# Optimization experiments

Hardware: AMD Instinct MI355X
Metric: run time of the kernel (lower is better)

Reference implementation:

```python
import jax, jax.numpy as jnp
import numpy as np

HID = 1024
NEG = -1e10


def setup_inputs() -> dict:
    key = jax.random.key(0)
    ks = jax.random.split(key, 8)
    batch, src_len = 64, 512
    hidden = jax.random.normal(ks[0], (batch, HID), dtype=jnp.float32)
    encoder_outputs = jax.random.normal(ks[1], (src_len, batch, 2 * HID), dtype=jnp.float32)
    mask = jax.random.randint(ks[2], (batch, src_len), 0, 2).astype(bool)
    # params (torch Linear: y = x @ W.T + b)
    sW = 1.0 / np.sqrt(HID)
    sU = 1.0 / np.sqrt(2 * HID)
    W_w = jax.random.uniform(ks[3], (HID, HID), jnp.float32, -sW, sW)
    W_b = jax.random.uniform(ks[4], (HID,), jnp.float32, -sW, sW)
    U_w = jax.random.uniform(ks[5], (HID, 2 * HID), jnp.float32, -sU, sU)
    U_b = jax.random.uniform(ks[6], (HID,), jnp.float32, -sU, sU)
    v_w = jax.random.uniform(ks[7], (1, HID), jnp.float32, -sW, sW)
    return {"hidden": hidden, "encoder_outputs": encoder_outputs, "mask": mask,
            "W_w": W_w, "W_b": W_b, "U_w": U_w, "U_b": U_b, "v_w": v_w}


def reference(hidden, encoder_outputs, mask, W_w, W_b, U_w, U_b, v_w):
    # hidden: [B, H]; encoder_outputs: [S, B, 2H]; mask: [B, S]
    Wh = hidden @ W_w.T + W_b                       # [B, H], broadcast over S
    enc = jnp.transpose(encoder_outputs, (1, 0, 2))  # [B, S, 2H]
    Ue = jnp.einsum('bse,he->bsh', enc, U_w) + U_b   # [B, S, H]
    energy = jnp.tanh(Wh[:, None, :] + Ue) @ v_w[0]  # [B, S]
    energy = jnp.where(mask, NEG, energy)
    return jax.nn.softmax(energy, axis=1)
```

## Files before the change

### kernel.cpp

```cpp
#include <hip/hip_runtime.h>
#include <math.h>

#define HID   1024
#define HID2  2048
#define BATCH 64
#define SRC   512
#define MROWS (SRC * BATCH)
#define NEGV  (-1e10f)

typedef int  i4v __attribute__((ext_vector_type(4)));
typedef float f4v __attribute__((ext_vector_type(4)));

__global__ void zero_energy(float* __restrict__ e) {
    int i = blockIdx.x * 256 + threadIdx.x;
    if (i < MROWS) e[i] = 0.f;
}

__global__ void split_i8(const float* __restrict__ src,
                         signed char* __restrict__ q1b,
                         signed char* __restrict__ q2b,
                         int n16, float s1, float inv_s1, float s2) {
    int i = blockIdx.x * 256 + threadIdx.x;
    if (i >= n16) return;
    const float4* s = (const float4*)src + (size_t)i * 4;
    float v[16];
    *(float4*)&v[0]  = s[0];
    *(float4*)&v[4]  = s[1];
    *(float4*)&v[8]  = s[2];
    *(float4*)&v[12] = s[3];
    unsigned w1[4], w2[4];
#pragma unroll
    for (int p = 0; p < 4; ++p) {
        unsigned a1 = 0, a2 = 0;
#pragma unroll
        for (int j = 0; j < 4; ++j) {
            float a  = v[p * 4 + j];
            float q1 = rintf(a * s1);
            q1 = fminf(fmaxf(q1, -127.f), 127.f);
            float r  = fmaf(q1, -inv_s1, a);
            float q2 = rintf(r * s2);
            q2 = fminf(fmaxf(q2, -127.f), 127.f);
            a1 |= ((unsigned)((int)q1 & 0xff)) << (8 * j);
            a2 |= ((unsigned)((int)q2 & 0xff)) << (8 * j);
        }
        w1[p] = a1; w2[p] = a2;
    }
    ((uint4*)q1b)[i] = make_uint4(w1[0], w1[1], w1[2], w1[3]);
    ((uint4*)q2b)[i] = make_uint4(w2[0], w2[1], w2[2], w2[3]);
}

__global__ void quant_i8(const float* __restrict__ src,
                         signed char* __restrict__ qb,
                         int n16, float s) {
    int i = blockIdx.x * 256 + threadIdx.x;
    if (i >= n16) return;
    const float4* sp = (const float4*)src + (size_t)i * 4;
    float v[16];
    *(float4*)&v[0]  = sp[0];
    *(float4*)&v[4]  = sp[1];
    *(float4*)&v[8]  = sp[2];
    *(float4*)&v[12] = sp[3];
    unsigned w[4];
#pragma unroll
    for (int p = 0; p < 4; ++p) {
        unsigned a = 0;
#pragma unroll
        for (int j = 0; j < 4; ++j) {
            float q = rintf(v[p * 4 + j] * s);
            q = fminf(fmaxf(q, -127.f), 127.f);
            a |= ((unsigned)((int)q & 0xff)) << (8 * j);
        }
        w[p] = a;
    }
    ((uint4*)qb)[i] = make_uint4(w[0], w[1], w[2], w[3]);
}

__global__ void wh_kernel(const float* __restrict__ hidden,
                          const float* __restrict__ W_w,
                          const float* __restrict__ W_b,
                          float* __restrict__ Wh) {
    __shared__ float sh[HID];
    const int b = blockIdx.y;
    const int t = threadIdx.x;
    for (int k = t; k < HID; k += 256) sh[k] = hidden[b * HID + k];
    __syncthreads();
    const int h = blockIdx.x * 256 + t;
    const float* wr = W_w + (size_t)h * HID;
    float acc = 0.f;
    for (int k = 0; k < HID; k += 4) {
        float4 w = *(const float4*)(wr + k);
        acc += sh[k] * w.x + sh[k+1] * w.y + sh[k+2] * w.z + sh[k+3] * w.w;
    }
    Wh[b * HID + h] = acc + W_b[h];
}

static __device__ __forceinline__ float tanh_fast(float x) {
    float ax = fabsf(x);
    float t  = __expf(-2.f * ax);
    float r  = __fdividef(1.f - t, 1.f + t);
    return copysignf(r, x);
}

__global__ __launch_bounds__(256, 2)
void gemm_energy(const signed char* __restrict__ A1,
                 const signed char* __restrict__ A2,
                 const signed char* __restrict__ B1,
                 const float* __restrict__ Ub,
                 const float* __restrict__ vw,
                 const float* __restrict__ Wh,
                 float* __restrict__ energy,
                 int m_base)
{
    __shared__ signed char sAll[2 * 3 * 8192];

    const int tid  = threadIdx.x;
    const int wave = tid >> 6;
    const int lane = tid & 63;

    const int nwg = (int)(gridDim.x * gridDim.y);
    const int bid = (int)(blockIdx.y * gridDim.x + blockIdx.x);
    const int cpx = nwg >> 3;
    const int swz = (bid & 7) * cpx + (bid >> 3);
    const int h0 = (swz & 7) * 128;
    const int m0 = (swz >> 3) * 128;

    const int wm = wave & 1;
    const int wn = wave >> 1;

    i4v c1[4][4], c2[4][4];
#pragma unroll
    for (int i = 0; i < 4; i++)
#pragma unroll
        for (int j = 0; j < 4; j++) {
            c1[i][j] = (i4v){0, 0, 0, 0};
            c2[i][j] = (i4v){0, 0, 0, 0};
        }

    const int ar = lane & 15;
    const int ko = (((lane >> 4) ^ ((ar >> 1) & 3)) * 16);

#define STAGE_TILES(CB, K0)                                                   \
    {                                                                         \
        _Pragma("unroll")                                                     \
        for (int it = 0; it < 2; ++it) {                                      \
            const int f    = it * 256 + tid;                                  \
            const int row  = f >> 2;                                          \
            const int inn  = (((f & 3) ^ ((row >> 1) & 3))) * 16;             \
            const int loff = (CB) + (it * 256 + wave * 64) * 16;              \
            const signed char* ga = A1 + (size_t)(m0 + row) * HID2 + (K0) + inn; \
            __builtin_amdgcn_global_load_lds(                                 \
                (const __attribute__((address_space(1))) unsigned int*)ga,    \
                (__attribute__((address_space(3))) unsigned int*)(sAll + loff), \
                16, 0, 0);                                                    \
            const signed char* gb = A2 + (size_t)(m0 + row) * HID2 + (K0) + inn; \
            __builtin_amdgcn_global_load_lds(                                 \
                (const __attribute__((address_space(1))) unsigned int*)gb,    \
                (__attribute__((address_space(3))) unsigned int*)(sAll + 8192 + loff), \
                16, 0, 0);                                                    \
            const signed char* gc = B1 + (size_t)(h0 + row) * HID2 + (K0) + inn; \
            __builtin_amdgcn_global_load_lds(                                 \
                (const __attribute__((address_space(1))) unsigned int*)gc,    \
                (__attribute__((address_space(3))) unsigned int*)(sAll + 16384 + loff), \
                16, 0, 0);                                                    \
        }                                                                     \
    }

    STAGE_TILES(0, 0);
    asm volatile("s_waitcnt vmcnt(0)" ::: "memory");
    __builtin_amdgcn_s_barrier();

    int cur = 0;
    for (int ks = 0; ks < 32; ++ks) {
        const int cb = cur * 24576;
        if (ks + 1 < 32) STAGE_TILES(cb ^ 24576, (ks + 1) * 64);

        i4v a1[4], a2[4], b1[4];
#pragma unroll
        for (int i = 0; i < 4; ++i) {
            const int ra = cb + (wm * 64 + i * 16 + ar) * 64 + ko;
            const int rb = cb + 16384 + (wn * 64 + i * 16 + ar) * 64 + ko;
            a1[i] = *(const i4v*)&sAll[ra];
            a2[i] = *(const i4v*)&sAll[8192 + ra];
            b1[i] = *(const i4v*)&sAll[rb];
        }
        asm volatile("s_waitcnt lgkmcnt(0)" ::: "memory");
        __builtin_amdgcn_sched_barrier(0);

        __builtin_amdgcn_s_setprio(1);
#pragma unroll
        for (int i = 0; i < 4; ++i)
#pragma unroll
            for (int j = 0; j < 4; ++j) {
                c1[i][j] = __builtin_amdgcn_mfma_i32_16x16x64_i8(a1[i], b1[j], c1[i][j], 0, 0, 0);
                c2[i][j] = __builtin_amdgcn_mfma_i32_16x16x64_i8(a2[i], b1[j], c2[i][j], 0, 0, 0);
            }
        __builtin_amdgcn_s_setprio(0);

        asm volatile("s_waitcnt vmcnt(0)" ::: "memory");
        __builtin_amdgcn_s_barrier();
        cur ^= 1;
    }
#undef STAGE_TILES

    const int col = lane & 15;
    const int rg  = lane >> 4;
    const float invs = 1.f / (4096.f * 5746.f);
    float vj[4], ubj[4];
#pragma unroll
    for (int j = 0; j < 4; ++j) {
        const int hc = h0 + wn * 64 + j * 16 + col;
        vj[j]  = vw[hc];
        ubj[j] = Ub[hc];
    }
#pragma unroll
    for (int i = 0; i < 4; ++i) {
#pragma unroll
        for (int r = 0; r < 4; ++r) {
            const int mm = m0 + wm * 64 + i * 16 + rg * 4 + r;
            const int b  = (m_base + mm) & 63;
            const float* whr = Wh + b * HID + h0 + wn * 64 + col;
            float e = 0.f;
#pragma unroll
            for (int j = 0; j < 4; ++j) {
                float C = fmaf((float)c1[i][j][r], 256.f, (float)c2[i][j][r]) * invs;
                float x = C + ubj[j] + whr[j * 16];
                e += vj[j] * tanh_fast(x);
            }
            e += __shfl_xor(e, 1, 64);
            e += __shfl_xor(e, 2, 64);
            e += __shfl_xor(e, 4, 64);
            e += __shfl_xor(e, 8, 64);
            if (col == 0) atomicAdd(&energy[m_base + mm], e);
        }
    }
}

__global__ void softmax_kernel(const float* __restrict__ energy,
                               const int* __restrict__ mask,
                               float* __restrict__ out) {
    const int b = blockIdx.x;
    const int t = threadIdx.x;
    __shared__ float wmax[4], wsum[4];

    float x0 = energy[t * 64 + b];
    float x1 = energy[(t + 256) * 64 + b];
    float e0 = mask[b * SRC + t]       ? NEGV : x0;
    float e1 = mask[b * SRC + t + 256] ? NEGV : x1;

    float mx = fmaxf(e0, e1);
#pragma unroll
    for (int off = 1; off < 64; off <<= 1)
        mx = fmaxf(mx, __shfl_xor(mx, off, 64));
    const int wid = t >> 6, lane = t & 63;
    if (lane == 0) wmax[wid] = mx;
    __syncthreads();
    mx = fmaxf(fmaxf(wmax[0], wmax[1]), fmaxf(wmax[2], wmax[3]));

    float p0 = expf(e0 - mx), p1 = expf(e1 - mx);
    float sum = p0 + p1;
#pragma unroll
    for (int off = 1; off < 64; off <<= 1)
        sum += __shfl_xor(sum, off, 64);
    if (lane == 0) wsum[wid] = sum;
    __syncthreads();
    sum = wsum[0] + wsum[1] + wsum[2] + wsum[3];
    const float inv = 1.f / sum;
    out[b * SRC + t]       = p0 * inv;
    out[b * SRC + t + 256] = p1 * inv;
}

extern "C" void kernel_launch(void* const* d_in, const int* in_sizes, int n_in,
                              void* d_out, int out_size, void* d_ws, size_t ws_size,
                              hipStream_t stream) {
    const float* hidden = (const float*)d_in[0];
    const float* enc    = (const float*)d_in[1];
    const int*   mask   = (const int*)d_in[2];
    const float* W_w    = (const float*)d_in[3];
    const float* W_b    = (const float*)d_in[4];
    const float* U_w    = (const float*)d_in[5];
    const float* U_b    = (const float*)d_in[6];
    const float* v_w    = (const float*)d_in[7];
    float* out = (float*)d_out;

    char* p = (char*)d_ws;
    float* Wh     = (float*)p;             p += (size_t)BATCH * HID * 4;
    float* energy = (float*)p;             p += (size_t)MROWS * 4;
    signed char* B1 = (signed char*)p;     p += (size_t)HID * HID2;
    const size_t fixed = (size_t)(p - (char*)d_ws);

    int R = 1024;
    const int cand[6] = {32768, 16384, 8192, 4096, 2048, 1024};
    for (int c = 0; c < 6; ++c) {
        if (fixed + (size_t)cand[c] * HID2 * 2 <= ws_size) { R = cand[c]; break; }
    }
    signed char* A1 = (signed char*)p;
    signed char* A2 = A1 + (size_t)R * HID2;

    const float Sa1 = 16.f, iSa1 = 1.f / 16.f, Sa2 = 4096.f;
    const float Sb1 = 5746.f;

    hipLaunchKernelGGL(zero_energy, dim3(MROWS / 256), dim3(256), 0, stream, energy);
    hipLaunchKernelGGL(wh_kernel, dim3(4, BATCH), dim3(256), 0, stream,
                       hidden, W_w, W_b, Wh);
    {
        const int n16 = HID * HID2 / 16;
        hipLaunchKernelGGL(quant_i8, dim3((n16 + 255) / 256), dim3(256), 0, stream,
                           U_w, B1, n16, Sb1);
    }
    for (int c0 = 0; c0 < MROWS; c0 += R) {
        const int n16 = R * HID2 / 16;
        hipLaunchKernelGGL(split_i8, dim3((n16 + 255) / 256), dim3(256), 0, stream,
                           enc + (size_t)c0 * HID2, A1, A2, n16, Sa1, iSa1, Sa2);
        hipLaunchKernelGGL(gemm_energy, dim3(HID / 128, R / 128), dim3(256), 0, stream,
                           A1, A2, B1, U_b, v_w, Wh, energy, c0);
    }
    hipLaunchKernelGGL(softmax_kernel, dim3(BATCH), dim3(256), 0, stream,
                       energy, mask, out);
}
```

Before: 604.0 us.

## Triple-buffer GEMM LDS tiles and use grid-stride coalesced quantization kernels

The int8 GEMM moves from double to triple buffering in shared memory. Tiles are prefetched two K-steps ahead, and the barrier waits with vmcnt(6) so the next stage's loads stay in flight. The setprio and sched_barrier hints are removed. The quantization kernels become grid-stride loops that handle one float4 per thread per iteration with fixed grid sizes, which gives coalesced narrow stores. Raising shared memory to 72KB per block may reduce occupancy below the two blocks per CU that the launch bounds request.

```diff
diff --git a/kernel.cpp b/kernel.cpp
--- a/kernel.cpp
+++ b/kernel.cpp
@@ -19,22 +19,17 @@
 __global__ void split_i8(const float* __restrict__ src,
                          signed char* __restrict__ q1b,
                          signed char* __restrict__ q2b,
-                         int n16, float s1, float inv_s1, float s2) {
-    int i = blockIdx.x * 256 + threadIdx.x;
-    if (i >= n16) return;
-    const float4* s = (const float4*)src + (size_t)i * 4;
-    float v[16];
-    *(float4*)&v[0]  = s[0];
-    *(float4*)&v[4]  = s[1];
-    *(float4*)&v[8]  = s[2];
-    *(float4*)&v[12] = s[3];
-    unsigned w1[4], w2[4];
-#pragma unroll
-    for (int p = 0; p < 4; ++p) {
+                         int n4, float s1, float inv_s1, float s2) {
+    const float4* s4 = (const float4*)src;
+    unsigned* o1 = (unsigned*)q1b;
+    unsigned* o2 = (unsigned*)q2b;
+    for (int i = blockIdx.x * 256 + threadIdx.x; i < n4; i += gridDim.x * 256) {
+        float4 v = s4[i];
+        float vv[4] = {v.x, v.y, v.z, v.w};
         unsigned a1 = 0, a2 = 0;
 #pragma unroll
         for (int j = 0; j < 4; ++j) {
-            float a  = v[p * 4 + j];
+            float a  = vv[j];
             float q1 = rintf(a * s1);
             q1 = fminf(fmaxf(q1, -127.f), 127.f);
             float r  = fmaf(q1, -inv_s1, a);
@@ -43,36 +38,28 @@
             a1 |= ((unsigned)((int)q1 & 0xff)) << (8 * j);
             a2 |= ((unsigned)((int)q2 & 0xff)) << (8 * j);
         }
-        w1[p] = a1; w2[p] = a2;
-    }
-    ((uint4*)q1b)[i] = make_uint4(w1[0], w1[1], w1[2], w1[3]);
-    ((uint4*)q2b)[i] = make_uint4(w2[0], w2[1], w2[2], w2[3]);
+        o1[i] = a1;
+        o2[i] = a2;
+    }
 }
 
 __global__ void quant_i8(const float* __restrict__ src,
                          signed char* __restrict__ qb,
-                         int n16, float s) {
-    int i = blockIdx.x * 256 + threadIdx.x;
-    if (i >= n16) return;
-    const float4* sp = (const float4*)src + (size_t)i * 4;
-    float v[16];
-    *(float4*)&v[0]  = sp[0];
-    *(float4*)&v[4]  = sp[1];
-    *(float4*)&v[8]  = sp[2];
-    *(float4*)&v[12] = sp[3];
-    unsigned w[4];
-#pragma unroll
-    for (int p = 0; p < 4; ++p) {
+                         int n4, float s) {
+    const float4* s4 = (const float4*)src;
+    unsigned* o = (unsigned*)qb;
+    for (int i = blockIdx.x * 256 + threadIdx.x; i < n4; i += gridDim.x * 256) {
+        float4 v = s4[i];
+        float vv[4] = {v.x, v.y, v.z, v.w};
         unsigned a = 0;
 #pragma unroll
         for (int j = 0; j < 4; ++j) {
-            float q = rintf(v[p * 4 + j] * s);
+            float q = rintf(vv[j] * s);
             q = fminf(fmaxf(q, -127.f), 127.f);
             a |= ((unsigned)((int)q & 0xff)) << (8 * j);
         }
-        w[p] = a;
-    }
-    ((uint4*)qb)[i] = make_uint4(w[0], w[1], w[2], w[3]);
+        o[i] = a;
+    }
 }
 
 __global__ void wh_kernel(const float* __restrict__ hidden,
@@ -111,7 +98,7 @@
                  float* __restrict__ energy,
                  int m_base)
 {
-    __shared__ signed char sAll[2 * 3 * 8192];
+    __shared__ signed char sAll[3 * 3 * 8192];
 
     const int tid  = threadIdx.x;
     const int wave = tid >> 6;
@@ -165,28 +152,26 @@
         }                                                                     \
     }
 
+#define SYNC_KEEP6() asm volatile("s_waitcnt vmcnt(6) lgkmcnt(0)\n\ts_barrier" ::: "memory")
+#define SYNC_DRAIN() asm volatile("s_waitcnt vmcnt(0) lgkmcnt(0)\n\ts_barrier" ::: "memory")
+
     STAGE_TILES(0, 0);
-    asm volatile("s_waitcnt vmcnt(0)" ::: "memory");
-    __builtin_amdgcn_s_barrier();
-
-    int cur = 0;
+    STAGE_TILES(24576, 64);
+    SYNC_KEEP6();
+
+    int pv = 2 * 24576, cu = 0, nx = 24576;
     for (int ks = 0; ks < 32; ++ks) {
-        const int cb = cur * 24576;
-        if (ks + 1 < 32) STAGE_TILES(cb ^ 24576, (ks + 1) * 64);
+        if (ks < 30) STAGE_TILES(pv, (ks + 2) * 64);
 
         i4v a1[4], a2[4], b1[4];
 #pragma unroll
         for (int i = 0; i < 4; ++i) {
-            const int ra = cb + (wm * 64 + i * 16 + ar) * 64 + ko;
-            const int rb = cb + 16384 + (wn * 64 + i * 16 + ar) * 64 + ko;
+            const int ra = cu + (wm * 64 + i * 16 + ar) * 64 + ko;
+            const int rb = cu + 16384 + (wn * 64 + i * 16 + ar) * 64 + ko;
             a1[i] = *(const i4v*)&sAll[ra];
             a2[i] = *(const i4v*)&sAll[8192 + ra];
             b1[i] = *(const i4v*)&sAll[rb];
         }
-        asm volatile("s_waitcnt lgkmcnt(0)" ::: "memory");
-        __builtin_amdgcn_sched_barrier(0);
-
-        __builtin_amdgcn_s_setprio(1);
 #pragma unroll
         for (int i = 0; i < 4; ++i)
 #pragma unroll
@@ -194,13 +179,13 @@
                 c1[i][j] = __builtin_amdgcn_mfma_i32_16x16x64_i8(a1[i], b1[j], c1[i][j], 0, 0, 0);
                 c2[i][j] = __builtin_amdgcn_mfma_i32_16x16x64_i8(a2[i], b1[j], c2[i][j], 0, 0, 0);
             }
-        __builtin_amdgcn_s_setprio(0);
-
-        asm volatile("s_waitcnt vmcnt(0)" ::: "memory");
-        __builtin_amdgcn_s_barrier();
-        cur ^= 1;
+
+        if (ks < 30) SYNC_KEEP6(); else SYNC_DRAIN();
+        const int t = cu; cu = nx; nx = pv; pv = t;
     }
 #undef STAGE_TILES
+#undef SYNC_KEEP6
+#undef SYNC_DRAIN
 
     const int col = lane & 15;
     const int rg  = lane >> 4;
@@ -303,14 +288,14 @@
     hipLaunchKernelGGL(wh_kernel, dim3(4, BATCH), dim3(256), 0, stream,
                        hidden, W_w, W_b, Wh);
     {
-        const int n16 = HID * HID2 / 16;
-        hipLaunchKernelGGL(quant_i8, dim3((n16 + 255) / 256), dim3(256), 0, stream,
-                           U_w, B1, n16, Sb1);
+        const int n4 = HID * HID2 / 4;
+        hipLaunchKernelGGL(quant_i8, dim3(1024), dim3(256), 0, stream,
+                           U_w, B1, n4, Sb1);
     }
     for (int c0 = 0; c0 < MROWS; c0 += R) {
-        const int n16 = R * HID2 / 16;
-        hipLaunchKernelGGL(split_i8, dim3((n16 + 255) / 256), dim3(256), 0, stream,
-                           enc + (size_t)c0 * HID2, A1, A2, n16, Sa1, iSa1, Sa2);
+        const int n4 = R * HID2 / 4;
+        hipLaunchKernelGGL(split_i8, dim3(2048), dim3(256), 0, stream,
+                           enc + (size_t)c0 * HID2, A1, A2, n4, Sa1, iSa1, Sa2);
         hipLaunchKernelGGL(gemm_energy, dim3(HID / 128, R / 128), dim3(256), 0, stream,
                            A1, A2, B1, U_b, v_w, Wh, energy, c0);
     }
```

New measurement: 595.7 us. About the same (-1.4%).
